# Kernel tuning notes

Measured on AMD Instinct MI355X. Metric: run time of the kernel, lower is better.

The kernel has to match this reference:

```python
import jax, jax.numpy as jnp
import numpy as np

MARGIN = 0.2
PRED_RATE = 1.0
MAX_VIOLATION = True


def t2i_score(images, obj_nums, captions, cap_lens):
    """images: (Bi, O, D); captions: (Bc, W, D).
    For each image, keep only its first obj_nums[i] objects, compute all
    object-word similarities vs every caption, max-pool over objects,
    sum over all W words (incl. padding, as in the torch code), and
    normalize by caption length. Returns (Bi, Bc)."""
    O = images.shape[1]
    # dot[i, c, o, w] = <images[i, o], captions[c, w]>
    dot = jnp.einsum('iod,cwd->icow', images, captions)
    valid = jnp.arange(O)[None, :] < obj_nums[:, None]          # (Bi, O)
    dot = jnp.where(valid[:, None, :, None], dot, -jnp.inf)
    pooled = dot.max(axis=2).sum(axis=2)                        # (Bi, Bc)
    return pooled / cap_lens.astype(pooled.dtype)[None, :]


def setup_inputs() -> dict:
    key = jax.random.key(0)
    ks = jax.random.split(key, 10)
    B, O, W, D = 128, 36, 50, 128
    Op, Wp = 25, 30
    return {
        'im':         jax.random.normal(ks[0], (B, O, D), dtype=jnp.float32),
        'im_l':       jax.random.randint(ks[1], (B,), 1, O + 1, dtype=jnp.int32),
        's':          jax.random.normal(ks[2], (B, W, D), dtype=jnp.float32),
        's_l':        jax.random.randint(ks[3], (B,), 1, W + 1, dtype=jnp.int32),
        'pred':       jax.random.normal(ks[4], (B, Op, D), dtype=jnp.float32),
        'pred_l':     jax.random.randint(ks[5], (B,), 1, Op + 1, dtype=jnp.int32),
        'cap_o_pred': jax.random.normal(ks[6], (B, Op, D), dtype=jnp.float32),
        'cap_o_l':    jax.random.randint(ks[7], (B,), 1, Op + 1, dtype=jnp.int32),
        'c_r_pred':   jax.random.normal(ks[8], (B, Wp, D), dtype=jnp.float32),
        'c_r_l':      jax.random.randint(ks[9], (B,), 1, Wp + 1, dtype=jnp.int32),
    }


def reference(im, im_l, s, s_l, pred, pred_l, cap_o_pred, cap_o_l, c_r_pred, c_r_l):
    scores = (t2i_score(im, im_l, s, s_l)
              + PRED_RATE * t2i_score(pred, pred_l, c_r_pred, c_r_l))  # (B, B)
    B = scores.shape[0]
    diag = jnp.diagonal(scores)
    cost_s = jnp.maximum(MARGIN + scores - diag[:, None], 0.0)
    cost_im = jnp.maximum(MARGIN + scores - diag[None, :], 0.0)
    eye = jnp.eye(B, dtype=bool)
    cost_s = jnp.where(eye, 0.0, cost_s)
    cost_im = jnp.where(eye, 0.0, cost_im)
    if MAX_VIOLATION:
        cost_s = cost_s.max(axis=1)
        cost_im = cost_im.max(axis=0)
    return cost_s.sum() + cost_im.sum()
```

## Files before the change

kernel.cpp:

```cpp
#include <hip/hip_runtime.h>

typedef __bf16 bf16x8 __attribute__((ext_vector_type(8)));
typedef float f32x4 __attribute__((ext_vector_type(4)));
typedef unsigned int u32x4 __attribute__((ext_vector_type(4)));

__device__ __forceinline__ unsigned short f2bf(float f) {
  unsigned int u = __float_as_uint(f);
  u += 0x7FFFu + ((u >> 16) & 1u);
  return (unsigned short)(u >> 16);
}

__device__ __forceinline__ bf16x8 load_frag(const unsigned short* p) {
  u32x4 v = *(const u32x4*)p;
  return __builtin_bit_cast(bf16x8, v);
}

__device__ __forceinline__ void keep(bf16x8& x) {
  asm volatile("" : "+v"(x));
}

__global__ __launch_bounds__(256) void convert_all(
    const float* __restrict__ im, const float* __restrict__ s,
    const float* __restrict__ pred, const float* __restrict__ crp,
    unsigned short* __restrict__ imb, unsigned short* __restrict__ sb,
    unsigned short* __restrict__ pb, unsigned short* __restrict__ cb)
{
  int b = blockIdx.x;
  const float* src; unsigned short* dst; int O, OP, base;
  if (b < 768)       { src = im;   dst = imb; O = 36; OP = 48; base = 0; }
  else if (b < 1568) { src = s;    dst = sb;  O = 50; OP = 50; base = 768; }
  else if (b < 2080) { src = pred; dst = pb;  O = 25; OP = 32; base = 1568; }
  else               { src = crp;  dst = cb;  O = 30; OP = 30; base = 2080; }
  int tid = (b - base) * 256 + (int)threadIdx.x;
  int total = 128 * OP * 32;
  if (tid >= total) return;
  int d4 = tid & 31;
  int o  = (tid >> 5) % OP;
  int bb = tid / (OP * 32);
  unsigned short r0 = 0, r1 = 0, r2 = 0, r3 = 0;
  if (o < O) {
    const float4 v = *(const float4*)(src + ((bb * O + o) << 7) + (d4 << 2));
    r0 = f2bf(v.x); r1 = f2bf(v.y); r2 = f2bf(v.z); r3 = f2bf(v.w);
  }
  ushort4 outv; outv.x = r0; outv.y = r1; outv.z = r2; outv.w = r3;
  *(ushort4*)(dst + (size_t)tid * 4) = outv;
}

template<int MT, int W>
__device__ __forceinline__ void t2i_im2(
    const unsigned short* __restrict__ A,
    const unsigned short* __restrict__ Bw,
    const int* __restrict__ obj_l, const int* __restrict__ cap_l,
    float* __restrict__ pooled,
    int vb, float* wmax)
{
  const int ig  = vb >> 3;
  const int i0  = ig * 2;
  const int cg0 = (vb & 7) * 16;
  const int tid = threadIdx.x;
  const int wv = tid >> 6, lane = tid & 63;
  const int quad = lane >> 4, n16 = lane & 15;
  const int ol0 = obj_l[i0], ol1 = obj_l[i0 + 1];

  bf16x8 af[2][MT][4];
#pragma unroll
  for (int im = 0; im < 2; ++im) {
    const unsigned short* Ab =
        A + (((size_t)(i0 + im) * (MT * 16) + n16) << 7) + quad * 8;
#pragma unroll
    for (int t = 0; t < MT; ++t)
#pragma unroll
      for (int sf = 0; sf < 4; ++sf)
        af[im][t][sf] = load_frag(Ab + ((t * 16) << 7) + sf * 32);
  }
#pragma unroll
  for (int im = 0; im < 2; ++im)
#pragma unroll
    for (int t = 0; t < MT; ++t)
#pragma unroll
      for (int sf = 0; sf < 4; ++sf)
        keep(af[im][t][sf]);

  const unsigned short* Bbase = Bw + (((size_t)cg0 * W + n16) << 7) + quad * 8;

  bf16x8 bcur[4];
  {
    const unsigned short* bp = Bbase + ((wv * 16) << 7);
#pragma unroll
    for (int sf = 0; sf < 4; ++sf) bcur[sf] = load_frag(bp + sf * 32);
  }

  for (int nt = wv; nt < W; nt += 4) {
    const int ntn = (nt + 4 < W) ? (nt + 4) : wv;
    const unsigned short* bpn = Bbase + ((ntn * 16) << 7);
    bf16x8 bnext[4];
#pragma unroll
    for (int sf = 0; sf < 4; ++sf) bnext[sf] = load_frag(bpn + sf * 32);

    f32x4 acc[2][MT];
#pragma unroll
    for (int im = 0; im < 2; ++im)
#pragma unroll
      for (int t = 0; t < MT; ++t) { f32x4 z = {0.f,0.f,0.f,0.f}; acc[im][t] = z; }
#pragma unroll
    for (int sf = 0; sf < 4; ++sf)
#pragma unroll
      for (int im = 0; im < 2; ++im)
#pragma unroll
        for (int t = 0; t < MT; ++t)
          acc[im][t] = __builtin_amdgcn_mfma_f32_16x16x32_bf16(
              af[im][t][sf], bcur[sf], acc[im][t], 0, 0, 0);

#pragma unroll
    for (int im = 0; im < 2; ++im) {
      const int ol = im ? ol1 : ol0;
      float m = -3.0e38f;
#pragma unroll
      for (int t = 0; t < MT; ++t)
#pragma unroll
        for (int r = 0; r < 4; ++r) {
          int o = t * 16 + quad * 4 + r;
          if (o < ol) m = fmaxf(m, acc[im][t][r]);
        }
      m = fmaxf(m, __shfl_xor(m, 16));
      m = fmaxf(m, __shfl_xor(m, 32));
      if (quad == 0) wmax[im * (16 * W) + nt * 16 + n16] = m;
    }

#pragma unroll
    for (int sf = 0; sf < 4; ++sf) bcur[sf] = bnext[sf];
  }
  __syncthreads();

  if (tid < 32) {
    const int im = tid >> 4, c = tid & 15;
    const float* wp = wmax + im * (16 * W) + c * W;
    float ssum = 0.f;
    for (int w = 0; w < W; ++w) ssum += wp[w];
    const int cc = cg0 + c;
    pooled[((i0 + im) << 7) + cc] = ssum / (float)cap_l[cc];
  }
}

__global__ __launch_bounds__(256, 2) void t2i_both(
    const unsigned short* __restrict__ imb, const unsigned short* __restrict__ sb,
    const unsigned short* __restrict__ pb,  const unsigned short* __restrict__ cb,
    const int* __restrict__ im_l, const int* __restrict__ s_l,
    const int* __restrict__ pred_l, const int* __restrict__ crl,
    float* __restrict__ p1, float* __restrict__ p2)
{
  __shared__ float wmax[2 * 16 * 50];
  t2i_im2<3, 50>(imb, sb, im_l, s_l, p1, (int)blockIdx.x, wmax);
  __syncthreads();
  t2i_im2<2, 30>(pb, cb, pred_l, crl, p2, (int)blockIdx.x, wmax);
}

__global__ __launch_bounds__(256) void loss_kernel(
    const float* __restrict__ p1, const float* __restrict__ p2,
    float* __restrict__ out)
{
  __shared__ float cmax[2][128];
  __shared__ float rmax[2][128];
  __shared__ float wsum[2];
  const int tid = threadIdx.x;
  const int h = tid >> 7, j = tid & 127;

  {
    float cm = -3.0e38f;
    for (int rr = 0; rr < 64; ++rr) {
      const int row = h * 64 + rr;
      const float v = p1[row * 128 + j] + p2[row * 128 + j];
      cm = (row == j) ? cm : fmaxf(cm, v);
    }
    cmax[h][j] = cm;
  }
  {
    float rm = -3.0e38f;
    for (int k = 0; k < 64; ++k) {
      const int c = h * 64 + k;
      const float v = p1[j * 128 + c] + p2[j * 128 + c];
      rm = (c == j) ? rm : fmaxf(rm, v);
    }
    rmax[h][j] = rm;
  }
  __syncthreads();

  float v = 0.f;
  if (tid < 128) {
    const float d  = p1[tid * 129] + p2[tid * 129];
    const float rm = fmaxf(rmax[0][tid], rmax[1][tid]);
    const float cm = fmaxf(cmax[0][tid], cmax[1][tid]);
    v = fmaxf(0.2f + rm - d, 0.f) + fmaxf(0.2f + cm - d, 0.f);
  }
#pragma unroll
  for (int o = 32; o; o >>= 1) v += __shfl_xor(v, o);
  if (tid == 0)  wsum[0] = v;
  if (tid == 64) wsum[1] = v;
  __syncthreads();
  if (tid == 0) out[0] = wsum[0] + wsum[1];
}

extern "C" void kernel_launch(void* const* d_in, const int* in_sizes, int n_in,
                              void* d_out, int out_size, void* d_ws, size_t ws_size,
                              hipStream_t stream)
{
  const float* im     = (const float*)d_in[0];
  const int*   im_l   = (const int*)  d_in[1];
  const float* s      = (const float*)d_in[2];
  const int*   s_l    = (const int*)  d_in[3];
  const float* pred   = (const float*)d_in[4];
  const int*   pred_l = (const int*)  d_in[5];
  const float* crp    = (const float*)d_in[8];
  const int*   crl    = (const int*)  d_in[9];

  char* ws = (char*)d_ws;
  const size_t off_imb = 0;
  const size_t off_sb  = off_imb + (size_t)128 * 48 * 128 * 2;
  const size_t off_pb  = off_sb  + (size_t)128 * 50 * 128 * 2;
  const size_t off_cb  = off_pb  + (size_t)128 * 32 * 128 * 2;
  const size_t off_p1  = off_cb  + (size_t)128 * 30 * 128 * 2;
  const size_t off_p2  = off_p1  + (size_t)128 * 128 * 4;

  unsigned short* imb = (unsigned short*)(ws + off_imb);
  unsigned short* sb  = (unsigned short*)(ws + off_sb);
  unsigned short* pb  = (unsigned short*)(ws + off_pb);
  unsigned short* cb  = (unsigned short*)(ws + off_cb);
  float* p1 = (float*)(ws + off_p1);
  float* p2 = (float*)(ws + off_p2);

  hipLaunchKernelGGL(convert_all, dim3(2560), dim3(256), 0, stream,
                     im, s, pred, crp, imb, sb, pb, cb);
  hipLaunchKernelGGL(t2i_both, dim3(512), dim3(256), 0, stream,
                     imb, sb, pb, cb, im_l, s_l, pred_l, crl, p1, p2);
  hipLaunchKernelGGL(loss_kernel, dim3(1), dim3(256), 0, stream,
                     p1, p2, (float*)d_out);
}
```

Before: 139.6 us.

## Fuse fp32-to-bf16 conversion into MFMA kernel and split the two scores across blocks

Removes the separate conversion kernel. The t2i kernel now loads fp32 inputs directly and converts them to bf16 fragments in registers, masking padded objects with zeros. The two similarity computations, previously run back to back in each block, now go to separate blocks, doubling the grid to 1024. This drops one launch and the bf16 workspace round trip. In exchange the caption fragments are reloaded from fp32 (twice the bytes) and reconverted by every block that uses them.

```diff
diff --git a/kernel.cpp b/kernel.cpp
--- a/kernel.cpp
+++ b/kernel.cpp
@@ -10,8 +10,19 @@
   return (unsigned short)(u >> 16);
 }
 
-__device__ __forceinline__ bf16x8 load_frag(const unsigned short* p) {
-  u32x4 v = *(const u32x4*)p;
+__device__ __forceinline__ bf16x8 cvt8(const float* __restrict__ p) {
+  const float4 a = *(const float4*)p;
+  const float4 b = *(const float4*)(p + 4);
+  u32x4 v;
+  v.x = ((unsigned)f2bf(a.y) << 16) | (unsigned)f2bf(a.x);
+  v.y = ((unsigned)f2bf(a.w) << 16) | (unsigned)f2bf(a.z);
+  v.z = ((unsigned)f2bf(b.y) << 16) | (unsigned)f2bf(b.x);
+  v.w = ((unsigned)f2bf(b.w) << 16) | (unsigned)f2bf(b.z);
+  return __builtin_bit_cast(bf16x8, v);
+}
+
+__device__ __forceinline__ bf16x8 zero8() {
+  u32x4 v; v.x = 0; v.y = 0; v.z = 0; v.w = 0;
   return __builtin_bit_cast(bf16x8, v);
 }
 
@@ -19,43 +30,15 @@
   asm volatile("" : "+v"(x));
 }
 
-__global__ __launch_bounds__(256) void convert_all(
-    const float* __restrict__ im, const float* __restrict__ s,
-    const float* __restrict__ pred, const float* __restrict__ crp,
-    unsigned short* __restrict__ imb, unsigned short* __restrict__ sb,
-    unsigned short* __restrict__ pb, unsigned short* __restrict__ cb)
-{
-  int b = blockIdx.x;
-  const float* src; unsigned short* dst; int O, OP, base;
-  if (b < 768)       { src = im;   dst = imb; O = 36; OP = 48; base = 0; }
-  else if (b < 1568) { src = s;    dst = sb;  O = 50; OP = 50; base = 768; }
-  else if (b < 2080) { src = pred; dst = pb;  O = 25; OP = 32; base = 1568; }
-  else               { src = crp;  dst = cb;  O = 30; OP = 30; base = 2080; }
-  int tid = (b - base) * 256 + (int)threadIdx.x;
-  int total = 128 * OP * 32;
-  if (tid >= total) return;
-  int d4 = tid & 31;
-  int o  = (tid >> 5) % OP;
-  int bb = tid / (OP * 32);
-  unsigned short r0 = 0, r1 = 0, r2 = 0, r3 = 0;
-  if (o < O) {
-    const float4 v = *(const float4*)(src + ((bb * O + o) << 7) + (d4 << 2));
-    r0 = f2bf(v.x); r1 = f2bf(v.y); r2 = f2bf(v.z); r3 = f2bf(v.w);
-  }
-  ushort4 outv; outv.x = r0; outv.y = r1; outv.z = r2; outv.w = r3;
-  *(ushort4*)(dst + (size_t)tid * 4) = outv;
-}
-
-template<int MT, int W>
+template<int MT, int W, int O>
 __device__ __forceinline__ void t2i_im2(
-    const unsigned short* __restrict__ A,
-    const unsigned short* __restrict__ Bw,
+    const float* __restrict__ A,
+    const float* __restrict__ Bw,
     const int* __restrict__ obj_l, const int* __restrict__ cap_l,
     float* __restrict__ pooled,
     int vb, float* wmax)
 {
-  const int ig  = vb >> 3;
-  const int i0  = ig * 2;
+  const int i0  = (vb >> 3) * 2;
   const int cg0 = (vb & 7) * 16;
   const int tid = threadIdx.x;
   const int wv = tid >> 6, lane = tid & 63;
@@ -64,15 +47,16 @@
 
   bf16x8 af[2][MT][4];
 #pragma unroll
-  for (int im = 0; im < 2; ++im) {
-    const unsigned short* Ab =
-        A + (((size_t)(i0 + im) * (MT * 16) + n16) << 7) + quad * 8;
-#pragma unroll
-    for (int t = 0; t < MT; ++t)
+  for (int im = 0; im < 2; ++im)
+#pragma unroll
+    for (int t = 0; t < MT; ++t) {
+      const int o = t * 16 + n16;
 #pragma unroll
       for (int sf = 0; sf < 4; ++sf)
-        af[im][t][sf] = load_frag(Ab + ((t * 16) << 7) + sf * 32);
-  }
+        af[im][t][sf] = (o < O)
+            ? cvt8(A + (((size_t)(i0 + im) * O + o) << 7) + quad * 8 + sf * 32)
+            : zero8();
+    }
 #pragma unroll
   for (int im = 0; im < 2; ++im)
 #pragma unroll
@@ -81,21 +65,21 @@
       for (int sf = 0; sf < 4; ++sf)
         keep(af[im][t][sf]);
 
-  const unsigned short* Bbase = Bw + (((size_t)cg0 * W + n16) << 7) + quad * 8;
+  const float* Bbase = Bw + (((size_t)cg0 * W + n16) << 7) + quad * 8;
 
   bf16x8 bcur[4];
   {
-    const unsigned short* bp = Bbase + ((wv * 16) << 7);
-#pragma unroll
-    for (int sf = 0; sf < 4; ++sf) bcur[sf] = load_frag(bp + sf * 32);
+    const float* bp = Bbase + ((size_t)(wv * 16) << 7);
+#pragma unroll
+    for (int sf = 0; sf < 4; ++sf) bcur[sf] = cvt8(bp + sf * 32);
   }
 
   for (int nt = wv; nt < W; nt += 4) {
     const int ntn = (nt + 4 < W) ? (nt + 4) : wv;
-    const unsigned short* bpn = Bbase + ((ntn * 16) << 7);
+    const float* bpn = Bbase + ((size_t)(ntn * 16) << 7);
     bf16x8 bnext[4];
 #pragma unroll
-    for (int sf = 0; sf < 4; ++sf) bnext[sf] = load_frag(bpn + sf * 32);
+    for (int sf = 0; sf < 4; ++sf) bnext[sf] = cvt8(bpn + sf * 32);
 
     f32x4 acc[2][MT];
 #pragma unroll
@@ -142,17 +126,18 @@
   }
 }
 
-__global__ __launch_bounds__(256, 2) void t2i_both(
-    const unsigned short* __restrict__ imb, const unsigned short* __restrict__ sb,
-    const unsigned short* __restrict__ pb,  const unsigned short* __restrict__ cb,
+__global__ __launch_bounds__(256, 2) void t2i_fused(
+    const float* __restrict__ im,   const float* __restrict__ s,
+    const float* __restrict__ pred, const float* __restrict__ crp,
     const int* __restrict__ im_l, const int* __restrict__ s_l,
     const int* __restrict__ pred_l, const int* __restrict__ crl,
     float* __restrict__ p1, float* __restrict__ p2)
 {
   __shared__ float wmax[2 * 16 * 50];
-  t2i_im2<3, 50>(imb, sb, im_l, s_l, p1, (int)blockIdx.x, wmax);
-  __syncthreads();
-  t2i_im2<2, 30>(pb, cb, pred_l, crl, p2, (int)blockIdx.x, wmax);
+  if (blockIdx.x < 512)
+    t2i_im2<3, 50, 36>(im, s, im_l, s_l, p1, (int)blockIdx.x, wmax);
+  else
+    t2i_im2<2, 30, 25>(pred, crp, pred_l, crl, p2, (int)blockIdx.x - 512, wmax);
 }
 
 __global__ __launch_bounds__(256) void loss_kernel(
@@ -214,24 +199,11 @@
   const int*   crl    = (const int*)  d_in[9];
 
   char* ws = (char*)d_ws;
-  const size_t off_imb = 0;
-  const size_t off_sb  = off_imb + (size_t)128 * 48 * 128 * 2;
-  const size_t off_pb  = off_sb  + (size_t)128 * 50 * 128 * 2;
-  const size_t off_cb  = off_pb  + (size_t)128 * 32 * 128 * 2;
-  const size_t off_p1  = off_cb  + (size_t)128 * 30 * 128 * 2;
-  const size_t off_p2  = off_p1  + (size_t)128 * 128 * 4;
-
-  unsigned short* imb = (unsigned short*)(ws + off_imb);
-  unsigned short* sb  = (unsigned short*)(ws + off_sb);
-  unsigned short* pb  = (unsigned short*)(ws + off_pb);
-  unsigned short* cb  = (unsigned short*)(ws + off_cb);
-  float* p1 = (float*)(ws + off_p1);
-  float* p2 = (float*)(ws + off_p2);
-
-  hipLaunchKernelGGL(convert_all, dim3(2560), dim3(256), 0, stream,
-                     im, s, pred, crp, imb, sb, pb, cb);
-  hipLaunchKernelGGL(t2i_both, dim3(512), dim3(256), 0, stream,
-                     imb, sb, pb, cb, im_l, s_l, pred_l, crl, p1, p2);
+  float* p1 = (float*)ws;
+  float* p2 = (float*)(ws + (size_t)128 * 128 * 4);
+
+  hipLaunchKernelGGL(t2i_fused, dim3(1024), dim3(256), 0, stream,
+                     im, s, pred, crp, im_l, s_l, pred_l, crl, p1, p2);
   hipLaunchKernelGGL(loss_kernel, dim3(1), dim3(256), 0, stream,
                      p1, p2, (float*)d_out);
 }
```

New measurement: 162.9 us. +16.7%, slower.

## Split t2i sub-problems across separate blocks and deepen B-fragment prefetch

Applied to the files above, without the earlier changes.

The fused scoring kernel used to run the image/caption pass and the predicate pass one after the other inside each block. Now it launches twice as many blocks, and each block handles only one pass. Separately, the word-tile loop is fully unrolled with a compile-time trip count and a three-slot register buffer, so B fragments are prefetched two iterations ahead. Waves whose tile index runs past W wrap around and recompute early tiles, rewriting the same values to shared memory. The aim is more parallelism across CUs and better hiding of global-load latency, at the cost of a few redundant MFMA iterations and higher register pressure.

```diff
diff --git a/kernel.cpp b/kernel.cpp
--- a/kernel.cpp
+++ b/kernel.cpp
@@ -46,7 +46,7 @@
   *(ushort4*)(dst + (size_t)tid * 4) = outv;
 }
 
-template<int MT, int W>
+template<int MT, int W, int NITER>
 __device__ __forceinline__ void t2i_im2(
     const unsigned short* __restrict__ A,
     const unsigned short* __restrict__ Bw,
@@ -54,8 +54,7 @@
     float* __restrict__ pooled,
     int vb, float* wmax)
 {
-  const int ig  = vb >> 3;
-  const int i0  = ig * 2;
+  const int i0  = (vb >> 3) * 2;
   const int cg0 = (vb & 7) * 16;
   const int tid = threadIdx.x;
   const int wv = tid >> 6, lane = tid & 63;
@@ -83,19 +82,32 @@
 
   const unsigned short* Bbase = Bw + (((size_t)cg0 * W + n16) << 7) + quad * 8;
 
-  bf16x8 bcur[4];
+  auto ntof = [&](int it) {
+    int nt = wv + it * 4;
+    return (nt < W) ? nt : nt - W;
+  };
+
+  bf16x8 buf[3][4];
   {
-    const unsigned short* bp = Bbase + ((wv * 16) << 7);
-#pragma unroll
-    for (int sf = 0; sf < 4; ++sf) bcur[sf] = load_frag(bp + sf * 32);
-  }
-
-  for (int nt = wv; nt < W; nt += 4) {
-    const int ntn = (nt + 4 < W) ? (nt + 4) : wv;
-    const unsigned short* bpn = Bbase + ((ntn * 16) << 7);
-    bf16x8 bnext[4];
-#pragma unroll
-    for (int sf = 0; sf < 4; ++sf) bnext[sf] = load_frag(bpn + sf * 32);
+    const unsigned short* p0 = Bbase + ((size_t)(ntof(0) * 16) << 7);
+#pragma unroll
+    for (int sf = 0; sf < 4; ++sf) buf[0][sf] = load_frag(p0 + sf * 32);
+  }
+  if (NITER > 1) {
+    const unsigned short* p1 = Bbase + ((size_t)(ntof(1) * 16) << 7);
+#pragma unroll
+    for (int sf = 0; sf < 4; ++sf) buf[1][sf] = load_frag(p1 + sf * 32);
+  }
+
+#pragma unroll
+  for (int it = 0; it < NITER; ++it) {
+    if (it + 2 < NITER) {
+      const unsigned short* pn = Bbase + ((size_t)(ntof(it + 2) * 16) << 7);
+#pragma unroll
+      for (int sf = 0; sf < 4; ++sf)
+        buf[(it + 2) % 3][sf] = load_frag(pn + sf * 32);
+    }
+    const int nt = ntof(it);
 
     f32x4 acc[2][MT];
 #pragma unroll
@@ -109,7 +121,7 @@
 #pragma unroll
         for (int t = 0; t < MT; ++t)
           acc[im][t] = __builtin_amdgcn_mfma_f32_16x16x32_bf16(
-              af[im][t][sf], bcur[sf], acc[im][t], 0, 0, 0);
+              af[im][t][sf], buf[it % 3][sf], acc[im][t], 0, 0, 0);
 
 #pragma unroll
     for (int im = 0; im < 2; ++im) {
@@ -126,9 +138,6 @@
       m = fmaxf(m, __shfl_xor(m, 32));
       if (quad == 0) wmax[im * (16 * W) + nt * 16 + n16] = m;
     }
-
-#pragma unroll
-    for (int sf = 0; sf < 4; ++sf) bcur[sf] = bnext[sf];
   }
   __syncthreads();
 
@@ -150,9 +159,10 @@
     float* __restrict__ p1, float* __restrict__ p2)
 {
   __shared__ float wmax[2 * 16 * 50];
-  t2i_im2<3, 50>(imb, sb, im_l, s_l, p1, (int)blockIdx.x, wmax);
-  __syncthreads();
-  t2i_im2<2, 30>(pb, cb, pred_l, crl, p2, (int)blockIdx.x, wmax);
+  if (blockIdx.x < 512)
+    t2i_im2<3, 50, 13>(imb, sb, im_l, s_l, p1, (int)blockIdx.x, wmax);
+  else
+    t2i_im2<2, 30, 8>(pb, cb, pred_l, crl, p2, (int)blockIdx.x - 512, wmax);
 }
 
 __global__ __launch_bounds__(256) void loss_kernel(
@@ -230,7 +240,7 @@
 
   hipLaunchKernelGGL(convert_all, dim3(2560), dim3(256), 0, stream,
                      im, s, pred, crp, imb, sb, pb, cb);
-  hipLaunchKernelGGL(t2i_both, dim3(512), dim3(256), 0, stream,
+  hipLaunchKernelGGL(t2i_both, dim3(1024), dim3(256), 0, stream,
                      imb, sb, pb, cb, im_l, s_l, pred_l, crl, p1, p2);
   hipLaunchKernelGGL(loss_kernel, dim3(1), dim3(256), 0, stream,
                      p1, p2, (float*)d_out);
```

After: 139.9 us. No clear change (+0.3%).
